# Kernel optimization log

Hardware: AMD Instinct MI355X
Metric: run time of the kernel (lower is better)

The kernel has to match this reference:

```python
import jax, jax.numpy as jnp
import numpy as np

N = 50000
E = 800000
P = 16
H = 128
NUM_LAYERS = 2


def _lin_params(key, fan_in, fan_out):
    k1, k2 = jax.random.split(key)
    bound = 1.0 / np.sqrt(fan_in)
    W = jax.random.uniform(k1, (fan_in, fan_out), jnp.float32, -bound, bound)
    b = jax.random.uniform(k2, (fan_out,), jnp.float32, -bound, bound)
    return W, b


def setup_inputs() -> dict:
    key = jax.random.key(0)
    ks = jax.random.split(key, 16)
    h = jax.random.normal(ks[0], (N, P), jnp.float32)
    x = jax.random.normal(ks[1], (N, 2), jnp.float32)
    edge_index = jax.random.randint(ks[2], (2, E), 0, N, jnp.int32)
    emb_W, emb_b = _lin_params(ks[3], P, H)
    e_W1, e_b1 = _lin_params(ks[4], 2 * H + 1, H)
    e_W2, e_b2 = _lin_params(ks[5], H, H)
    n_W1, n_b1 = _lin_params(ks[6], 2 * H, H)
    n_W2, n_b2 = _lin_params(ks[7], H, H)
    v_W1, v_b1 = _lin_params(ks[8], H, H)
    v_W2, v_b2 = _lin_params(ks[9], H, 2)
    c_W1, c_b1 = _lin_params(ks[10], H, H)
    c_W2, c_b2 = _lin_params(ks[11], H, 1)
    return dict(h=h, x=x, edge_index=edge_index,
                emb_W=emb_W, emb_b=emb_b,
                e_W1=e_W1, e_b1=e_b1, e_W2=e_W2, e_b2=e_b2,
                n_W1=n_W1, n_b1=n_b1, n_W2=n_W2, n_b2=n_b2,
                v_W1=v_W1, v_b1=v_b1, v_W2=v_W2, v_b2=v_b2,
                c_W1=c_W1, c_b1=c_b1, c_W2=c_W2, c_b2=c_b2)


def _mlp(z, W1, b1, W2, b2):
    return jnp.maximum(z @ W1 + b1, 0.0) @ W2 + b2


def reference(h, x, edge_index, emb_W, emb_b,
              e_W1, e_b1, e_W2, e_b2,
              n_W1, n_b1, n_W2, n_b2,
              v_W1, v_b1, v_W2, v_b2,
              c_W1, c_b1, c_W2, c_b2):
    row, col = edge_index[0], edge_index[1]
    n_nodes = h.shape[0]
    # edge count per source node for scatter-mean (0-count nodes stay 0)
    cnt = jax.ops.segment_sum(jnp.ones((row.shape[0],), h.dtype), row,
                              num_segments=n_nodes)
    denom = jnp.maximum(cnt, 1.0)[:, None]

    h = h @ emb_W + emb_b  # [N, H]
    v = None
    for _ in range(NUM_LAYERS):
        rel_pos = x[row] - x[col]                         # [E, 2]
        rel_dist = jnp.sum(rel_pos ** 2, axis=-1, keepdims=True)  # [E, 1]
        rel_theta = jnp.arctan2(rel_pos[:, 1], rel_pos[:, 0])     # [E]
        rel_pos2 = rel_dist * jnp.stack(
            [jnp.cos(2.0 * rel_theta), jnp.sin(2.0 * rel_theta)], axis=1)  # [E, 2]
        edge_feat = jnp.concatenate([h[row], h[col], rel_dist], axis=-1)   # [E, 2H+1]
        m_ij = _mlp(edge_feat, e_W1, e_b1, e_W2, e_b2)    # [E, H] (dropout = eval identity)
        m_i = jax.ops.segment_sum(m_ij, row, num_segments=n_nodes)  # [N, H]
        h = h + _mlp(jnp.concatenate([h, m_i], axis=-1), n_W1, n_b1, n_W2, n_b2)
        v = _mlp(h, v_W1, v_b1, v_W2, v_b2)               # [N, 2]
        coord = _mlp(m_ij, c_W1, c_b1, c_W2, c_b2)        # [E, 1]
        scat = jax.ops.segment_sum(rel_pos2 * coord, row, num_segments=n_nodes)
        v = v + scat / denom                              # scatter-mean
    # F.normalize(p=2, dim=-1, eps=1e-12)
    norm = jnp.linalg.norm(v, axis=-1, keepdims=True)
    v = v / jnp.maximum(norm, 1e-12)
    return h, x, v
```

## Files before the change

### kernel.cpp

```cpp
#include <hip/hip_runtime.h>

typedef _Float16 f16;
typedef unsigned short u16;
typedef f16 f16x2 __attribute__((ext_vector_type(2)));
typedef f16 f16x8 __attribute__((ext_vector_type(8)));
typedef float f32x4 __attribute__((ext_vector_type(4)));

constexpr int N_NODES = 50000;
constexpr int E_EDGES = 800000;
constexpr int NBINS   = 50176;
constexpr int NBLK    = 196;

constexpr size_t OFF_DEG   = 0;
constexpr size_t OFF_LOCEX = 200704;
constexpr size_t OFF_BSUM  = 401408;
constexpr size_t OFF_BOFF  = 402432;
constexpr size_t OFF_FILL  = 403456;
constexpr size_t OFF_SCAT  = 604160;
constexpr size_t OFF_SROW  = 1004160;
constexpr size_t OFF_SCOL  = 2604160;
constexpr size_t OFF_ZSUM  = 4204160;
constexpr size_t ZS_BYTES  = (size_t)N_NODES * 128 * 4;
constexpr size_t OFF_APRE  = OFF_ZSUM + ZS_BYTES;
constexpr size_t OFF_BPRE  = OFF_APRE + (size_t)N_NODES * 128 * 2;
constexpr size_t OFF_CMB   = OFF_BPRE + (size_t)N_NODES * 128 * 2;
constexpr size_t OFF_WX    = OFF_CMB + 65536;
constexpr size_t OFF_BVEC  = OFF_WX + 65536;
constexpr size_t OFF_BX    = OFF_BVEC + 512;
constexpr size_t OFF_WSWZ  = OFF_BX + 512;

__device__ __forceinline__ void split_f(float x, f16& h, f16& l) {
    h = (f16)x;
    l = (f16)(x - (float)h);
}

__device__ __forceinline__ f32x4 mfma3(f16x8 ah, f16x8 al, f16x8 bh, f16x8 bl, f32x4 acc) {
    acc = __builtin_amdgcn_mfma_f32_16x16x32_f16(ah, bh, acc, 0, 0, 0);
    acc = __builtin_amdgcn_mfma_f32_16x16x32_f16(al, bh, acc, 0, 0, 0);
    acc = __builtin_amdgcn_mfma_f32_16x16x32_f16(ah, bl, acc, 0, 0, 0);
    return acc;
}

__global__ __launch_bounds__(256) void compose_kernel(
    const float* __restrict__ eW2, const float* __restrict__ eb2,
    const float* __restrict__ nW1, const float* __restrict__ cW1,
    const float* __restrict__ cb1,
    float* __restrict__ Wcmb, float* __restrict__ Wx,
    float* __restrict__ bvec, float* __restrict__ bx)
{
    const int gid = blockIdx.x * 256 + threadIdx.x;
    if (gid < 16384) {
        const int k = gid >> 7, j = gid & 127;
        float s = 0.f;
        for (int t2 = 0; t2 < 128; ++t2) s += eW2[k * 128 + t2] * nW1[(128 + t2) * 128 + j];
        Wcmb[gid] = s;
    } else if (gid < 32768) {
        const int e = gid - 16384;
        const int k = e >> 7, j = e & 127;
        float s = 0.f;
        for (int t2 = 0; t2 < 128; ++t2) s += eW2[k * 128 + t2] * cW1[t2 * 128 + j];
        Wx[e] = s;
    } else if (gid < 32896) {
        const int j = gid - 32768;
        float s = 0.f;
        for (int k = 0; k < 128; ++k) s += eb2[k] * nW1[(128 + k) * 128 + j];
        bvec[j] = s;
    } else if (gid < 33024) {
        const int j = gid - 32896;
        float s = cb1[j];
        for (int k = 0; k < 128; ++k) s += eb2[k] * cW1[k * 128 + j];
        bx[j] = s;
    }
}

__global__ __launch_bounds__(256) void prep_kernel(
    const float* __restrict__ eW1, const float* __restrict__ nW1,
    const float* __restrict__ nW2, const float* __restrict__ vW1,
    const float* __restrict__ Wcmb, const float* __restrict__ Wx,
    f16* __restrict__ Wpres, f16* __restrict__ nW1cs,
    f16* __restrict__ nW2s, f16* __restrict__ vW1s, f16* __restrict__ Wxs)
{
    const int gid = blockIdx.x * 256 + threadIdx.x;
    int K32, e, which; f16* out;
    if (gid < 32768)       { which = 0; out = Wpres; K32 = 4; e = gid; }
    else if (gid < 65536)  { which = 1; out = nW1cs; K32 = 8; e = gid - 32768; }
    else if (gid < 81920)  { which = 2; out = nW2s;  K32 = 4; e = gid - 65536; }
    else if (gid < 98304)  { which = 3; out = vW1s;  K32 = 4; e = gid - 81920; }
    else                   { which = 4; out = Wxs;   K32 = 4; e = gid - 98304; }
    const int per = 512 * K32;
    const int ct = e / per, rem = e % per;
    const int kk = rem >> 9, lane = (rem >> 3) & 63, j = rem & 7;
    const int col = ct * 16 + (lane & 15);
    const int k = kk * 32 + ((lane >> 4) & 3) * 8 + j;
    float v;
    if (which == 0)      v = (col < 128) ? eW1[k * 128 + col] : eW1[(128 + k) * 128 + (col - 128)];
    else if (which == 1) v = (k < 128) ? nW1[k * 128 + col] : Wcmb[(k - 128) * 128 + col];
    else if (which == 2) v = nW2[k * 128 + col];
    else if (which == 3) v = vW1[k * 128 + col];
    else                 v = Wx[k * 128 + col];
    f16 h, l; split_f(v, h, l);
    const int base = ((ct * K32 + kk) * 2) * 512 + lane * 8 + j;
    out[base] = h;
    out[base + 512] = l;
}

__global__ __launch_bounds__(256) void hist_kernel(const int* __restrict__ eidx,
                                                   int* __restrict__ deg) {
    const int e = blockIdx.x * 256 + threadIdx.x;
    if (e < E_EDGES) atomicAdd(&deg[eidx[e]], 1);
}

__global__ __launch_bounds__(256) void scan1_kernel(const int* __restrict__ deg,
                                                    int* __restrict__ locEx,
                                                    int* __restrict__ blockSum) {
    __shared__ int s[256];
    const int t = threadIdx.x;
    const int gid = blockIdx.x * 256 + t;
    const int v = deg[gid];
    s[t] = v;
    __syncthreads();
    for (int off = 1; off < 256; off <<= 1) {
        const int add = (t >= off) ? s[t - off] : 0;
        __syncthreads();
        s[t] += add;
        __syncthreads();
    }
    locEx[gid] = s[t] - v;
    if (t == 255) blockSum[blockIdx.x] = s[255];
}

__global__ __launch_bounds__(256) void scan2_kernel(const int* __restrict__ blockSum,
                                                    int* __restrict__ blockOff) {
    __shared__ int s[256];
    const int t = threadIdx.x;
    const int v = (t < NBLK) ? blockSum[t] : 0;
    s[t] = v;
    __syncthreads();
    for (int off = 1; off < 256; off <<= 1) {
        const int add = (t >= off) ? s[t - off] : 0;
        __syncthreads();
        s[t] += add;
        __syncthreads();
    }
    if (t < NBLK) blockOff[t] = s[t] - v;
}

__global__ __launch_bounds__(256) void scatter_kernel(const int* __restrict__ eidx,
        const int* __restrict__ locEx, const int* __restrict__ blockOff,
        int* __restrict__ fill, u16* __restrict__ srow, u16* __restrict__ scol) {
    const int e = blockIdx.x * 256 + threadIdx.x;
    if (e >= E_EDGES) return;
    const int r = eidx[e], c = eidx[E_EDGES + e];
    const int pos = blockOff[r >> 8] + locEx[r] + atomicAdd(&fill[r], 1);
    srow[pos] = (u16)r;
    scol[pos] = (u16)c;
}

__global__ __launch_bounds__(256) void embed_kernel(
    const float* __restrict__ h_in, const float* __restrict__ embW,
    const float* __restrict__ embb, float* __restrict__ h)
{
    const int gid = blockIdx.x * 256 + threadIdx.x;
    if (gid >= N_NODES * 128) return;
    const int n = gid >> 7, j = gid & 127;
    float s = embb[j];
#pragma unroll
    for (int p = 0; p < 16; ++p) s += h_in[n * 16 + p] * embW[p * 128 + j];
    h[gid] = s;
}

__device__ __forceinline__ void stage8(const float* src, f16* dst) {
    const float4 f0 = *(const float4*)src;
    const float4 f1 = *(const float4*)(src + 4);
    const float xs[8] = {f0.x, f0.y, f0.z, f0.w, f1.x, f1.y, f1.z, f1.w};
    f16x8 vh, vl;
#pragma unroll
    for (int i = 0; i < 8; ++i) { f16 hh, ll; split_f(xs[i], hh, ll); vh[i] = hh; vl[i] = ll; }
    *(f16x8*)dst = vh;
    *(f16x8*)(dst + 8) = vl;
}

__global__ __launch_bounds__(256, 4) void pre_kernel(
    const float* __restrict__ h, const f16* __restrict__ Wpres,
    const float* __restrict__ eb1,
    f16* __restrict__ Apre, f16* __restrict__ Bpre)
{
    constexpr int S = 264;
    __shared__ f16 smA[64 * S];
    const int t = threadIdx.x;
    const int base = blockIdx.x * 64;
    const int lane = t & 63, w = t >> 6, qq = lane >> 4, nn = lane & 15;

#pragma unroll
    for (int it = 0; it < 4; ++it) {
        const int idx = it * 256 + t;
        const int el = idx >> 4, seg = idx & 15;
        const int node = base + el;
        f16* dst = &smA[el * S + seg * 16];
        if (node < N_NODES) {
            stage8(h + (size_t)node * 128 + seg * 8, dst);
        } else {
            *(f16x8*)dst = (f16x8)(f16)0.f;
            *(f16x8*)(dst + 8) = (f16x8)(f16)0.f;
        }
    }
    __syncthreads();

#pragma unroll
    for (int half = 0; half < 2; ++half) {
        f32x4 acc[4][2] = {};
        for (int kk = 0; kk < 4; ++kk) {
            f16x8 Ah[4], Al[4];
#pragma unroll
            for (int rt = 0; rt < 4; ++rt) {
                const f16* ap = &smA[(rt * 16 + nn) * S + (kk * 4 + qq) * 16];
                Ah[rt] = *(const f16x8*)ap;
                Al[rt] = *(const f16x8*)(ap + 8);
            }
#pragma unroll
            for (int c = 0; c < 2; ++c) {
                const int ct = w * 4 + half * 2 + c;
                const f16* bp = Wpres + (size_t)((ct * 4 + kk) * 2) * 512 + lane * 8;
                const f16x8 Bh = *(const f16x8*)bp;
                const f16x8 Bl = *(const f16x8*)(bp + 512);
#pragma unroll
                for (int rt = 0; rt < 4; ++rt)
                    acc[rt][c] = mfma3(Ah[rt], Al[rt], Bh, Bl, acc[rt][c]);
            }
        }
#pragma unroll
        for (int c = 0; c < 2; ++c) {
            const int col = w * 64 + half * 32 + c * 16 + nn;
#pragma unroll
            for (int rt = 0; rt < 4; ++rt) {
#pragma unroll
                for (int r = 0; r < 4; ++r) {
                    const int el = rt * 16 + qq * 4 + r;
                    const int node = base + el;
                    if (node < N_NODES) {
                        const float v = acc[rt][c][r];
                        if (col < 128) Apre[(size_t)node * 128 + col] = (f16)(v + eb1[col]);
                        else           Bpre[(size_t)node * 128 + (col - 128)] = (f16)v;
                    }
                }
            }
        }
    }
}

__global__ __launch_bounds__(256, 8) void edge_z_kernel(
    const u16* __restrict__ srow, const u16* __restrict__ scol,
    const float* __restrict__ x,
    const f16* __restrict__ Apre, const f16* __restrict__ Bpre,
    const float* __restrict__ wlast,
    float* __restrict__ zsum)
{
    constexpr int S2 = 136;
    __shared__ f16 smZ[64 * S2];
    __shared__ int smRow[64], smCol[64];
    __shared__ float smRd[64];
    const int t = threadIdx.x;
    const int base = blockIdx.x * 64;
    if (t < 64) {
        const int e = base + t;
        const int r = (int)srow[e], c = (int)scol[e];
        smRow[t] = r; smCol[t] = c;
        const float dx = x[2 * r] - x[2 * c];
        const float dy = x[2 * r + 1] - x[2 * c + 1];
        smRd[t] = dx * dx + dy * dy;
    }
    __syncthreads();

    const int seg = t & 15;
    const float4 w0 = *(const float4*)(wlast + seg * 8);
    const float4 w1 = *(const float4*)(wlast + seg * 8 + 4);
    const float wl[8] = {w0.x, w0.y, w0.z, w0.w, w1.x, w1.y, w1.z, w1.w};
#pragma unroll
    for (int it = 0; it < 4; ++it) {
        const int el = it * 16 + (t >> 4);
        const int rn = smRow[el], cn = smCol[el];
        const f16x8 av = *(const f16x8*)(Apre + (size_t)rn * 128 + seg * 8);
        const f16x8 bv = *(const f16x8*)(Bpre + (size_t)cn * 128 + seg * 8);
        const float rd = smRd[el];
        f16x8 vz;
#pragma unroll
        for (int i = 0; i < 8; ++i)
            vz[i] = (f16)fmaxf((float)av[i] + (float)bv[i] + rd * wl[i], 0.f);
        *(f16x8*)&smZ[el * S2 + seg * 8] = vz;
    }
    __syncthreads();

    const int p = t & 63, g = t >> 6;
    float a0 = 0.f, a1 = 0.f;
    int prev = smRow[g * 16];
#pragma unroll
    for (int e = g * 16; e < g * 16 + 16; ++e) {
        const int rw = smRow[e];
        if (rw != prev) {
            atomicAdd(&zsum[(size_t)prev * 128 + 2 * p], a0);
            atomicAdd(&zsum[(size_t)prev * 128 + 2 * p + 1], a1);
            a0 = a1 = 0.f; prev = rw;
        }
        const f16x2 v = *(const f16x2*)&smZ[e * S2 + 2 * p];
        a0 += (float)v[0]; a1 += (float)v[1];
    }
    atomicAdd(&zsum[(size_t)prev * 128 + 2 * p], a0);
    atomicAdd(&zsum[(size_t)prev * 128 + 2 * p + 1], a1);
}

__global__ __launch_bounds__(256, 6) void edge_coord_kernel(
    const u16* __restrict__ srow, const u16* __restrict__ scol,
    const float* __restrict__ x,
    const f16* __restrict__ Apre, const f16* __restrict__ Bpre,
    const float* __restrict__ wlast,
    const f16* __restrict__ Wxs, const float* __restrict__ bx,
    const float* __restrict__ cW2, const float* __restrict__ cb2,
    float* __restrict__ zsum, float* __restrict__ scat)
{
    constexpr int S2 = 136;
    __shared__ f16 smZ[64 * S2];
    __shared__ int smRow[64], smCol[64];
    __shared__ float smRd[64], smP2x[64], smP2y[64];
    __shared__ float smPart[4][64];

    const int t = threadIdx.x;
    const int base = blockIdx.x * 64;
    const int lane = t & 63, w = t >> 6, qq = lane >> 4, nn = lane & 15;

    if (t < 64) {
        const int e = base + t;
        const int r = (int)srow[e], c = (int)scol[e];
        smRow[t] = r; smCol[t] = c;
        const float dx = x[2 * r] - x[2 * c];
        const float dy = x[2 * r + 1] - x[2 * c + 1];
        smRd[t] = dx * dx + dy * dy;
        smP2x[t] = dx * dx - dy * dy;
        smP2y[t] = 2.0f * dx * dy;
    }
    __syncthreads();

    {
        const int seg = t & 15;
        const float4 w0 = *(const float4*)(wlast + seg * 8);
        const float4 w1 = *(const float4*)(wlast + seg * 8 + 4);
        const float wl[8] = {w0.x, w0.y, w0.z, w0.w, w1.x, w1.y, w1.z, w1.w};
#pragma unroll
        for (int it = 0; it < 4; ++it) {
            const int el = it * 16 + (t >> 4);
            const int rn = smRow[el], cn = smCol[el];
            const f16x8 av = *(const f16x8*)(Apre + (size_t)rn * 128 + seg * 8);
            const f16x8 bv = *(const f16x8*)(Bpre + (size_t)cn * 128 + seg * 8);
            const float rd = smRd[el];
            f16x8 vz;
#pragma unroll
            for (int i = 0; i < 8; ++i)
                vz[i] = (f16)fmaxf((float)av[i] + (float)bv[i] + rd * wl[i], 0.f);
            *(f16x8*)&smZ[el * S2 + seg * 8] = vz;
        }
    }
    __syncthreads();

    {
        const int p = t & 63, g = t >> 6;
        float a0 = 0.f, a1 = 0.f;
        int prev = smRow[g * 16];
#pragma unroll
        for (int e = g * 16; e < g * 16 + 16; ++e) {
            const int rw = smRow[e];
            if (rw != prev) {
                atomicAdd(&zsum[(size_t)prev * 128 + 2 * p], a0);
                atomicAdd(&zsum[(size_t)prev * 128 + 2 * p + 1], a1);
                a0 = a1 = 0.f; prev = rw;
            }
            const f16x2 v = *(const f16x2*)&smZ[e * S2 + 2 * p];
            a0 += (float)v[0]; a1 += (float)v[1];
        }
        atomicAdd(&zsum[(size_t)prev * 128 + 2 * p], a0);
        atomicAdd(&zsum[(size_t)prev * 128 + 2 * p + 1], a1);
    }

    f32x4 acc3[4][2] = {};
    for (int kk = 0; kk < 4; ++kk) {
        f16x8 A[4];
#pragma unroll
        for (int rt = 0; rt < 4; ++rt)
            A[rt] = *(const f16x8*)&smZ[(rt * 16 + nn) * S2 + (kk * 4 + qq) * 8];
#pragma unroll
        for (int c = 0; c < 2; ++c) {
            const int ct = w * 2 + c;
            const f16x8 Bh = *(const f16x8*)(Wxs + (size_t)((ct * 4 + kk) * 2) * 512 + lane * 8);
#pragma unroll
            for (int rt = 0; rt < 4; ++rt)
                acc3[rt][c] = __builtin_amdgcn_mfma_f32_16x16x32_f16(A[rt], Bh, acc3[rt][c], 0, 0, 0);
        }
    }
    float p3[4][4];
#pragma unroll
    for (int rt = 0; rt < 4; ++rt)
#pragma unroll
        for (int r = 0; r < 4; ++r) p3[rt][r] = 0.f;
#pragma unroll
    for (int c = 0; c < 2; ++c) {
        const int col = w * 32 + c * 16 + nn;
        const float c1 = bx[col];
        const float w2 = cW2[col];
#pragma unroll
        for (int rt = 0; rt < 4; ++rt)
#pragma unroll
            for (int r = 0; r < 4; ++r)
                p3[rt][r] += fmaxf(acc3[rt][c][r] + c1, 0.f) * w2;
    }
#pragma unroll
    for (int off = 1; off < 16; off <<= 1)
#pragma unroll
        for (int rt = 0; rt < 4; ++rt)
#pragma unroll
            for (int r = 0; r < 4; ++r) p3[rt][r] += __shfl_xor(p3[rt][r], off);
    if (nn == 0) {
#pragma unroll
        for (int rt = 0; rt < 4; ++rt)
#pragma unroll
            for (int r = 0; r < 4; ++r)
                smPart[w][rt * 16 + qq * 4 + r] = p3[rt][r];
    }
    __syncthreads();
    if (t < 64) {
        const float co = smPart[0][t] + smPart[1][t] + smPart[2][t] + smPart[3][t] + cb2[0];
        const int rw = smRow[t];
        atomicAdd(&scat[2 * rw],     smP2x[t] * co);
        atomicAdd(&scat[2 * rw + 1], smP2y[t] * co);
    }
}

__global__ __launch_bounds__(256, 4) void node_kernel(
    float* __restrict__ h, float* __restrict__ zsum,
    const int* __restrict__ deg,
    const f16* __restrict__ nW1cs, const float* __restrict__ nb1,
    const float* __restrict__ bvec,
    const f16* __restrict__ nW2s, const float* __restrict__ nb2)
{
    constexpr int S = 264;
    __shared__ f16 smA[64 * S];
    __shared__ float smDeg[64];
    const int t = threadIdx.x;
    const int base = blockIdx.x * 64;
    const int lane = t & 63, w = t >> 6, qq = lane >> 4, nn = lane & 15;

    if (t < 64) smDeg[t] = (float)deg[base + t];

    f32x4 acc1[4][2] = {};
    for (int chunk = 0; chunk < 2; ++chunk) {
        if (chunk) __syncthreads();
#pragma unroll
        for (int it = 0; it < 4; ++it) {
            const int idx = it * 256 + t;
            const int el = idx >> 4, seg = idx & 15;
            const int node = base + el;
            f16* dst = &smA[el * S + seg * 16];
            if (node < N_NODES) {
                if (chunk == 0) {
                    stage8(h + (size_t)node * 128 + seg * 8, dst);
                } else {
                    float* src = zsum + (size_t)node * 128 + seg * 8;
                    stage8(src, dst);
                    const float4 zz = {0.f, 0.f, 0.f, 0.f};
                    *(float4*)src = zz;
                    *(float4*)(src + 4) = zz;
                }
            } else {
                *(f16x8*)dst = (f16x8)(f16)0.f;
                *(f16x8*)(dst + 8) = (f16x8)(f16)0.f;
            }
        }
        __syncthreads();
        for (int kk = 0; kk < 4; ++kk) {
            f16x8 Ah[4], Al[4];
#pragma unroll
            for (int rt = 0; rt < 4; ++rt) {
                const f16* ap = &smA[(rt * 16 + nn) * S + (kk * 4 + qq) * 16];
                Ah[rt] = *(const f16x8*)ap;
                Al[rt] = *(const f16x8*)(ap + 8);
            }
            const int kkg = chunk * 4 + kk;
#pragma unroll
            for (int c = 0; c < 2; ++c) {
                const int ct = w * 2 + c;
                const f16* bp = nW1cs + (size_t)((ct * 8 + kkg) * 2) * 512 + lane * 8;
                const f16x8 Bh = *(const f16x8*)bp;
                const f16x8 Bl = *(const f16x8*)(bp + 512);
#pragma unroll
                for (int rt = 0; rt < 4; ++rt)
                    acc1[rt][c] = mfma3(Ah[rt], Al[rt], Bh, Bl, acc1[rt][c]);
            }
        }
    }
    __syncthreads();
#pragma unroll
    for (int c = 0; c < 2; ++c) {
        const int col = w * 32 + c * 16 + nn;
        const float b1 = nb1[col];
        const float bv = bvec[col];
#pragma unroll
        for (int rt = 0; rt < 4; ++rt) {
#pragma unroll
            for (int r = 0; r < 4; ++r) {
                const int el = rt * 16 + qq * 4 + r;
                const float z = fmaxf(acc1[rt][c][r] + b1 + smDeg[el] * bv, 0.f);
                f16 zh, zl; split_f(z, zh, zl);
                f16* zp = &smA[el * S + (col >> 3) * 16 + (col & 7)];
                zp[0] = zh; zp[8] = zl;
            }
        }
    }
    __syncthreads();

    f32x4 acc2[4][2] = {};
    for (int kk = 0; kk < 4; ++kk) {
        f16x8 Ah[4], Al[4];
#pragma unroll
        for (int rt = 0; rt < 4; ++rt) {
            const f16* ap = &smA[(rt * 16 + nn) * S + (kk * 4 + qq) * 16];
            Ah[rt] = *(const f16x8*)ap;
            Al[rt] = *(const f16x8*)(ap + 8);
        }
#pragma unroll
        for (int c = 0; c < 2; ++c) {
            const int ct = w * 2 + c;
            const f16* bp = nW2s + (size_t)((ct * 4 + kk) * 2) * 512 + lane * 8;
            const f16x8 Bh = *(const f16x8*)bp;
            const f16x8 Bl = *(const f16x8*)(bp + 512);
#pragma unroll
            for (int rt = 0; rt < 4; ++rt)
                acc2[rt][c] = mfma3(Ah[rt], Al[rt], Bh, Bl, acc2[rt][c]);
        }
    }
#pragma unroll
    for (int c = 0; c < 2; ++c) {
        const int col = w * 32 + c * 16 + nn;
        const float b2 = nb2[col];
#pragma unroll
        for (int rt = 0; rt < 4; ++rt) {
#pragma unroll
            for (int r = 0; r < 4; ++r) {
                const int el = rt * 16 + qq * 4 + r;
                const int node = base + el;
                if (node < N_NODES) {
                    const size_t ix = (size_t)node * 128 + col;
                    h[ix] = h[ix] + acc2[rt][c][r] + b2;
                }
            }
        }
    }
}

__global__ __launch_bounds__(256, 4) void final_kernel(
    const float* __restrict__ h, const float* __restrict__ x,
    const f16* __restrict__ vW1s, const float* __restrict__ vb1,
    const float* __restrict__ vW2, const float* __restrict__ vb2,
    const float* __restrict__ scat, const int* __restrict__ deg,
    float* __restrict__ out)
{
    constexpr int S = 264;
    __shared__ f16 smA[64 * S];
    const int t = threadIdx.x;
    const int base = blockIdx.x * 64;
    const int lane = t & 63, w = t >> 6, qq = lane >> 4, nn = lane & 15;

#pragma unroll
    for (int it = 0; it < 4; ++it) {
        const int idx = it * 256 + t;
        const int el = idx >> 4, seg = idx & 15;
        const int node = base + el;
        f16* dst = &smA[el * S + seg * 16];
        if (node < N_NODES) {
            stage8(h + (size_t)node * 128 + seg * 8, dst);
        } else {
            *(f16x8*)dst = (f16x8)(f16)0.f;
            *(f16x8*)(dst + 8) = (f16x8)(f16)0.f;
        }
    }
    __syncthreads();

    f32x4 acc1[4][2] = {};
    for (int kk = 0; kk < 4; ++kk) {
        f16x8 Ah[4], Al[4];
#pragma unroll
        for (int rt = 0; rt < 4; ++rt) {
            const f16* ap = &smA[(rt * 16 + nn) * S + (kk * 4 + qq) * 16];
            Ah[rt] = *(const f16x8*)ap;
            Al[rt] = *(const f16x8*)(ap + 8);
        }
#pragma unroll
        for (int c = 0; c < 2; ++c) {
            const int ct = w * 2 + c;
            const f16* bp = vW1s + (size_t)((ct * 4 + kk) * 2) * 512 + lane * 8;
            const f16x8 Bh = *(const f16x8*)bp;
            const f16x8 Bl = *(const f16x8*)(bp + 512);
#pragma unroll
            for (int rt = 0; rt < 4; ++rt)
                acc1[rt][c] = mfma3(Ah[rt], Al[rt], Bh, Bl, acc1[rt][c]);
        }
    }
    __syncthreads();
#pragma unroll
    for (int c = 0; c < 2; ++c) {
        const int col = w * 32 + c * 16 + nn;
        const float b1 = vb1[col];
#pragma unroll
        for (int rt = 0; rt < 4; ++rt) {
#pragma unroll
            for (int r = 0; r < 4; ++r) {
                const int el = rt * 16 + qq * 4 + r;
                const float z = fmaxf(acc1[rt][c][r] + b1, 0.f);
                f16 zh, zl; split_f(z, zh, zl);
                f16* zp = &smA[el * S + (col >> 3) * 16 + (col & 7)];
                zp[0] = zh; zp[8] = zl;
            }
        }
    }
    __syncthreads();

    float* out_x = out + (size_t)N_NODES * 128;
    float* out_v = out_x + (size_t)N_NODES * 2;
    if (t < 128) {
        const int node = base + (t >> 1);
        if (node < N_NODES) out_x[node * 2 + (t & 1)] = x[node * 2 + (t & 1)];
    }
    if (t < 128) {
        const int rl = t >> 1, comp = t & 1;
        const int node = base + rl;
        float s = 0.f;
        if (node < N_NODES) {
            s = vb2[comp];
            for (int k = 0; k < 128; ++k) {
                const f16* zp = &smA[rl * S + (k >> 3) * 16 + (k & 7)];
                const float z = (float)zp[0] + (float)zp[8];
                s += z * vW2[k * 2 + comp];
            }
            const float dn = fmaxf((float)deg[node], 1.0f);
            s += scat[node * 2 + comp] / dn;
        }
        const float other = __shfl_xor(s, 1);
        if (node < N_NODES) {
            const float nrm = sqrtf(s * s + other * other);
            out_v[node * 2 + comp] = s / fmaxf(nrm, 1e-12f);
        }
    }
}

extern "C" void kernel_launch(void* const* d_in, const int* in_sizes, int n_in,
                              void* d_out, int out_size, void* d_ws, size_t ws_size,
                              hipStream_t stream) {
    const float* h_in = (const float*)d_in[0];
    const float* x    = (const float*)d_in[1];
    const int*   eidx = (const int*)d_in[2];
    const float* embW = (const float*)d_in[3];
    const float* embb = (const float*)d_in[4];
    const float* eW1  = (const float*)d_in[5];
    const float* eb1  = (const float*)d_in[6];
    const float* eW2  = (const float*)d_in[7];
    const float* eb2  = (const float*)d_in[8];
    const float* nW1  = (const float*)d_in[9];
    const float* nb1  = (const float*)d_in[10];
    const float* nW2  = (const float*)d_in[11];
    const float* nb2  = (const float*)d_in[12];
    const float* vW1  = (const float*)d_in[13];
    const float* vb1  = (const float*)d_in[14];
    const float* vW2  = (const float*)d_in[15];
    const float* vb2  = (const float*)d_in[16];
    const float* cW1  = (const float*)d_in[17];
    const float* cb1  = (const float*)d_in[18];
    const float* cW2  = (const float*)d_in[19];
    const float* cb2  = (const float*)d_in[20];

    char* ws = (char*)d_ws;
    int* deg    = (int*)(ws + OFF_DEG);
    int* locEx  = (int*)(ws + OFF_LOCEX);
    int* bsum   = (int*)(ws + OFF_BSUM);
    int* boff   = (int*)(ws + OFF_BOFF);
    int* fill   = (int*)(ws + OFF_FILL);
    float* scat = (float*)(ws + OFF_SCAT);
    u16* srow   = (u16*)(ws + OFF_SROW);
    u16* scol   = (u16*)(ws + OFF_SCOL);
    float* zsum = (float*)(ws + OFF_ZSUM);
    f16* Apre   = (f16*)(ws + OFF_APRE);
    f16* Bpre   = (f16*)(ws + OFF_BPRE);
    float* Wcmb = (float*)(ws + OFF_CMB);
    float* Wx   = (float*)(ws + OFF_WX);
    float* bvec = (float*)(ws + OFF_BVEC);
    float* bx   = (float*)(ws + OFF_BX);
    f16* Wpres  = (f16*)(ws + OFF_WSWZ);
    f16* nW1cs  = Wpres + 65536;
    f16* nW2s   = nW1cs + 65536;
    f16* vW1s   = nW2s + 32768;
    f16* Wxs    = vW1s + 32768;

    float* hcur = (float*)d_out;

    hipMemsetAsync(ws, 0, OFF_SROW, stream);
    hipMemsetAsync(zsum, 0, ZS_BYTES, stream);

    compose_kernel<<<129, 256, 0, stream>>>(eW2, eb2, nW1, cW1, cb1, Wcmb, Wx, bvec, bx);
    prep_kernel<<<448, 256, 0, stream>>>(eW1, nW1, nW2, vW1, Wcmb, Wx,
                                         Wpres, nW1cs, nW2s, vW1s, Wxs);
    hist_kernel<<<(E_EDGES + 255) / 256, 256, 0, stream>>>(eidx, deg);
    scan1_kernel<<<NBLK, 256, 0, stream>>>(deg, locEx, bsum);
    scan2_kernel<<<1, 256, 0, stream>>>(bsum, boff);
    scatter_kernel<<<(E_EDGES + 255) / 256, 256, 0, stream>>>(eidx, locEx, boff,
                                                              fill, srow, scol);
    embed_kernel<<<(N_NODES * 128 + 255) / 256, 256, 0, stream>>>(h_in, embW, embb, hcur);

    const float* wlast = eW1 + 256 * 128;

    pre_kernel<<<(N_NODES + 63) / 64, 256, 0, stream>>>(hcur, Wpres, eb1, Apre, Bpre);
    edge_z_kernel<<<E_EDGES / 64, 256, 0, stream>>>(srow, scol, x, Apre, Bpre, wlast, zsum);
    node_kernel<<<(N_NODES + 63) / 64, 256, 0, stream>>>(hcur, zsum, deg,
        nW1cs, nb1, bvec, nW2s, nb2);

    pre_kernel<<<(N_NODES + 63) / 64, 256, 0, stream>>>(hcur, Wpres, eb1, Apre, Bpre);
    edge_coord_kernel<<<E_EDGES / 64, 256, 0, stream>>>(srow, scol, x, Apre, Bpre, wlast,
        Wxs, bx, cW2, cb2, zsum, scat);
    node_kernel<<<(N_NODES + 63) / 64, 256, 0, stream>>>(hcur, zsum, deg,
        nW1cs, nb1, bvec, nW2s, nb2);

    final_kernel<<<(N_NODES + 63) / 64, 256, 0, stream>>>(hcur, x,
        vW1s, vb1, vW2, vb2, scat, deg, (float*)d_out);
}
```

Before: 658.7 us.

## Restructure edge_z kernel to accumulate per-thread in registers without shared staging

```diff
diff --git a/kernel.cpp b/kernel.cpp
--- a/kernel.cpp
+++ b/kernel.cpp
@@ -248,20 +248,18 @@
     }
 }
 
-__global__ __launch_bounds__(256, 8) void edge_z_kernel(
+__global__ __launch_bounds__(256, 4) void edge_z_kernel(
     const u16* __restrict__ srow, const u16* __restrict__ scol,
     const float* __restrict__ x,
     const f16* __restrict__ Apre, const f16* __restrict__ Bpre,
     const float* __restrict__ wlast,
     float* __restrict__ zsum)
 {
-    constexpr int S2 = 136;
-    __shared__ f16 smZ[64 * S2];
-    __shared__ int smRow[64], smCol[64];
-    __shared__ float smRd[64];
+    __shared__ int smRow[256], smCol[256];
+    __shared__ float smRd[256];
     const int t = threadIdx.x;
-    const int base = blockIdx.x * 64;
-    if (t < 64) {
+    const int base = blockIdx.x * 256;
+    {
         const int e = base + t;
         const int r = (int)srow[e], c = (int)scol[e];
         smRow[t] = r; smCol[t] = c;
@@ -271,44 +269,46 @@
     }
     __syncthreads();
 
-    const int seg = t & 15;
+    const int seg = t & 15, g = t >> 4;
     const float4 w0 = *(const float4*)(wlast + seg * 8);
     const float4 w1 = *(const float4*)(wlast + seg * 8 + 4);
     const float wl[8] = {w0.x, w0.y, w0.z, w0.w, w1.x, w1.y, w1.z, w1.w};
-#pragma unroll
-    for (int it = 0; it < 4; ++it) {
-        const int el = it * 16 + (t >> 4);
-        const int rn = smRow[el], cn = smCol[el];
-        const f16x8 av = *(const f16x8*)(Apre + (size_t)rn * 128 + seg * 8);
-        const f16x8 bv = *(const f16x8*)(Bpre + (size_t)cn * 128 + seg * 8);
-        const float rd = smRd[el];
-        f16x8 vz;
-#pragma unroll
-        for (int i = 0; i < 8; ++i)
-            vz[i] = (f16)fmaxf((float)av[i] + (float)bv[i] + rd * wl[i], 0.f);
-        *(f16x8*)&smZ[el * S2 + seg * 8] = vz;
-    }
-    __syncthreads();
-
-    const int p = t & 63, g = t >> 6;
-    float a0 = 0.f, a1 = 0.f;
+
+    float acc[8] = {0.f, 0.f, 0.f, 0.f, 0.f, 0.f, 0.f, 0.f};
     int prev = smRow[g * 16];
 #pragma unroll
-    for (int e = g * 16; e < g * 16 + 16; ++e) {
-        const int rw = smRow[e];
-        if (rw != prev) {
-            atomicAdd(&zsum[(size_t)prev * 128 + 2 * p], a0);
-            atomicAdd(&zsum[(size_t)prev * 128 + 2 * p + 1], a1);
-            a0 = a1 = 0.f; prev = rw;
-        }
-        const f16x2 v = *(const f16x2*)&smZ[e * S2 + 2 * p];
-        a0 += (float)v[0]; a1 += (float)v[1];
-    }
-    atomicAdd(&zsum[(size_t)prev * 128 + 2 * p], a0);
-    atomicAdd(&zsum[(size_t)prev * 128 + 2 * p + 1], a1);
-}
-
-__global__ __launch_bounds__(256, 6) void edge_coord_kernel(
+    for (int half = 0; half < 2; ++half) {
+        f16x8 AV[8], BV[8];
+#pragma unroll
+        for (int i = 0; i < 8; ++i) {
+            const int el = g * 16 + half * 8 + i;
+            AV[i] = *(const f16x8*)(Apre + (size_t)smRow[el] * 128 + seg * 8);
+            BV[i] = *(const f16x8*)(Bpre + (size_t)smCol[el] * 128 + seg * 8);
+        }
+#pragma unroll
+        for (int i = 0; i < 8; ++i) {
+            const int el = g * 16 + half * 8 + i;
+            const int rn = smRow[el];
+            if (rn != prev) {
+#pragma unroll
+                for (int j = 0; j < 8; ++j)
+                    atomicAdd(&zsum[(size_t)prev * 128 + seg * 8 + j], acc[j]);
+#pragma unroll
+                for (int j = 0; j < 8; ++j) acc[j] = 0.f;
+                prev = rn;
+            }
+            const float rd = smRd[el];
+#pragma unroll
+            for (int j = 0; j < 8; ++j)
+                acc[j] += fmaxf((float)AV[i][j] + (float)BV[i][j] + rd * wl[j], 0.f);
+        }
+    }
+#pragma unroll
+    for (int j = 0; j < 8; ++j)
+        atomicAdd(&zsum[(size_t)prev * 128 + seg * 8 + j], acc[j]);
+}
+
+__global__ __launch_bounds__(256, 8) void edge_coord_kernel(
     const u16* __restrict__ srow, const u16* __restrict__ scol,
     const float* __restrict__ x,
     const f16* __restrict__ Apre, const f16* __restrict__ Bpre,
@@ -713,7 +713,7 @@
     const float* wlast = eW1 + 256 * 128;
 
     pre_kernel<<<(N_NODES + 63) / 64, 256, 0, stream>>>(hcur, Wpres, eb1, Apre, Bpre);
-    edge_z_kernel<<<E_EDGES / 64, 256, 0, stream>>>(srow, scol, x, Apre, Bpre, wlast, zsum);
+    edge_z_kernel<<<E_EDGES / 256, 256, 0, stream>>>(srow, scol, x, Apre, Bpre, wlast, zsum);
     node_kernel<<<(N_NODES + 63) / 64, 256, 0, stream>>>(hcur, zsum, deg,
         nW1cs, nb1, bvec, nW2s, nb2);
 
```

Result: slower. 950.4 us (+44.3%).
